# Optimization experiments

Hardware: AMD Instinct MI355X
Metric: run time of the kernel (lower is better)

## Reference

```python
import jax, jax.numpy as jnp
import numpy as np

NPG = 400          # nodes per graph (CC400 atlas ROIs)
B = 512            # graphs per batch
N = B * NPG        # total nodes
EPG = 6400         # edges per graph (avg degree 16)
E = B * EPG
F_IN = 200         # node feature dim
H = 64             # hidden_channels
C = 2              # num_classes


def _lin(k, fi, fo):
    return jax.random.normal(k, (fi, fo), jnp.float32) / np.sqrt(fi)


def setup_inputs() -> dict:
    key = jax.random.key(0)
    ks = jax.random.split(key, 16)
    # intra-graph edges: local src/dst in [0, NPG) plus per-graph offset
    g = jnp.repeat(jnp.arange(B, dtype=jnp.int32), EPG)
    src = jax.random.randint(ks[0], (E,), 0, NPG, dtype=jnp.int32) + g * NPG
    dst = jax.random.randint(ks[1], (E,), 0, NPG, dtype=jnp.int32) + g * NPG
    edge_index = jnp.stack([src, dst])  # [2, E]
    x = jax.random.normal(ks[2], (N, F_IN), jnp.float32)
    return dict(
        x=x, edge_index=edge_index, npg=NPG,
        # SAGEConv i: out = lin_l(mean_agg) + lin_r(x); lin_l carries the bias
        W1l=_lin(ks[3], F_IN, H), W1r=_lin(ks[4], F_IN, H), b1=jnp.zeros((H,), jnp.float32),
        W2l=_lin(ks[5], H, H), W2r=_lin(ks[6], H, H), b2=jnp.zeros((H,), jnp.float32),
        W3l=_lin(ks[7], H, H), W3r=_lin(ks[8], H, H), b3=jnp.zeros((H,), jnp.float32),
        # SAGPooling score GNN = GraphConv(H, 1): lin_rel(sum_agg) + lin_root(x)
        Wpr=_lin(ks[9], H, 1), bpr=jnp.zeros((1,), jnp.float32), Wpo=_lin(ks[10], H, 1),
        # final classifier
        Wlin=_lin(ks[11], H, C), blin=jnp.zeros((C,), jnp.float32),
    )


def reference(x, edge_index, npg, W1l, W1r, b1, W2l, W2r, b2, W3l, W3r, b3,
              Wpr, bpr, Wpo, Wlin, blin):
    n = x.shape[0]
    src, dst = edge_index[0], edge_index[1]

    deg = jax.ops.segment_sum(jnp.ones((src.shape[0],), x.dtype), dst, num_segments=n)
    inv_deg = 1.0 / jnp.maximum(deg, 1.0)  # [n]

    def sage(h, Wl, Wr, b):
        # mean aggregation over incoming edges, then lin_l(agg)+b + lin_r(h)
        agg = jax.ops.segment_sum(h[src], dst, num_segments=n) * inv_deg[:, None]
        return agg @ Wl + b + h @ Wr

    x1 = jax.nn.relu(sage(x, W1l, W1r, b1))
    x2 = jax.nn.relu(sage(x1, W2l, W2r, b2)) + x1
    x3 = jax.nn.relu(sage(x2, W3l, W3r, b3)) + x2

    # SAGPooling score via GraphConv (add aggregation)
    score = (jax.ops.segment_sum(x3[src], dst, num_segments=n) @ Wpr + bpr
             + x3 @ Wpo)[:, 0]  # [n]

    nb = n // npg            # number of graphs
    k = npg // 2             # ratio = 0.5, uniform graph sizes
    vals, idx = jax.lax.top_k(score.reshape(nb, npg), k)       # [nb, k]
    flat_idx = (jnp.arange(nb, dtype=idx.dtype)[:, None] * npg + idx).reshape(-1)
    xp = x3[flat_idx] * jnp.tanh(vals.reshape(-1))[:, None]    # [nb*k, H]

    pooled = xp.reshape(nb, k, -1).mean(axis=1)                # global_mean_pool
    logits = pooled @ Wlin + blin
    return jax.nn.log_softmax(logits, axis=1)
```

## Files before the change

### kernel.cpp

```cpp
#include <hip/hip_runtime.h>
#include <hip/hip_bf16.h>
#include <math.h>

#define F_IN 200
#define HDIM 64
#define NPG  400
#define EPG  6400
#define KSEL 200

typedef __attribute__((ext_vector_type(4))) float f32x4;
typedef __attribute__((ext_vector_type(8))) short s16x8;

__device__ __forceinline__ void gload_lds16(const void* g, void* l) {
    __builtin_amdgcn_global_load_lds(
        (const __attribute__((address_space(1))) void*)g,
        (__attribute__((address_space(3))) void*)l, 16, 0, 0);
}

__device__ __forceinline__ unsigned int bf16_rne(float x) {
    unsigned int b = __float_as_uint(x);
    return (b + 0x7FFFu + ((b >> 16) & 1u)) >> 16;
}

__device__ __forceinline__ void split8(f32x4 v0, f32x4 v1, s16x8& h, s16x8& l) {
    float x[8] = {v0.x, v0.y, v0.z, v0.w, v1.x, v1.y, v1.z, v1.w};
#pragma unroll
    for (int j = 0; j < 8; j++) {
        unsigned int hb = bf16_rne(x[j]);
        float hf = __uint_as_float(hb << 16);
        float r = x[j] - hf;
        unsigned int lb = bf16_rne(r);
        h[j] = (short)hb;
        l[j] = (short)lb;
    }
}

__global__ void pack_wf(const float* __restrict__ Wl, const float* __restrict__ Wr,
                        short* __restrict__ WF, int K, int KC) {
    int idx = blockIdx.x * blockDim.x + threadIdx.x;
    if (idx >= KC * 4096) return;
    int j    = idx & 7;
    int lane = (idx >> 3) & 63;
    int nf   = (idx >> 9) & 7;
    int kc   = idx >> 12;
    int k = kc * 32 + (lane >> 4) * 8 + j;
    int n = nf * 16 + (lane & 15);
    float v = 0.f;
    if (k < K) v = (n < 64) ? Wl[k * 64 + n] : Wr[k * 64 + (n - 64)];
    unsigned int hb = bf16_rne(v);
    float hf = __uint_as_float(hb << 16);
    unsigned int lb = bf16_rne(v - hf);
    WF[(size_t)((kc * 8 + nf) * 2 + 0) * 512 + lane * 8 + j] = (short)hb;
    WF[(size_t)((kc * 8 + nf) * 2 + 1) * 512 + lane * 8 + j] = (short)lb;
}

__global__ void pack_wf4(const float* __restrict__ Wl, const float* __restrict__ Wr,
                         short* __restrict__ WF) {
    int idx = blockIdx.x * blockDim.x + threadIdx.x;
    if (idx >= 4 * 2048) return;
    int j    = idx & 7;
    int lane = (idx >> 3) & 63;
    int nf   = (idx >> 9) & 3;
    int kc   = idx >> 11;
    int k = kc * 32 + (lane >> 4) * 8 + j;
    int n = nf * 16 + (lane & 15);
    float v = (k < 64) ? Wl[k * 64 + n] : Wr[(k - 64) * 64 + n];
    unsigned int hb = bf16_rne(v);
    float hf = __uint_as_float(hb << 16);
    unsigned int lb = bf16_rne(v - hf);
    WF[(size_t)((kc * 4 + nf) * 2 + 0) * 512 + lane * 8 + j] = (short)hb;
    WF[(size_t)((kc * 4 + nf) * 2 + 1) * 512 + lane * 8 + j] = (short)lb;
}

template <int K, int LDX, int KC, int TAIL>
__global__ __launch_bounds__(256) void gemm_lds(const float* __restrict__ X,
                                                const short* __restrict__ WF,
                                                float* __restrict__ O) {
    __shared__ float Xs[2][128 * 32];
    __shared__ short Ws[2][8 * 2 * 512];
    const int tid  = threadIdx.x;
    const int lane = tid & 63;
    const int wave = tid >> 6;
    const size_t rowbase = (size_t)blockIdx.x * 128;
    const f32x4 zero4 = (f32x4){0.f, 0.f, 0.f, 0.f};

    const int srow_off = wave * 32 + (lane >> 3);
    const int sbyte    = 16 * ((lane & 7) ^ (lane >> 3));

#define DMA_CHUNK(b, kc_) {                                                      \
    _Pragma("unroll")                                                            \
    for (int j = 0; j < 4; j++) {                                                \
        const char* xsrc = (const char*)X +                                      \
            (rowbase + srow_off + j * 8) * (size_t)(LDX * 4) + (kc_) * 128 + sbyte; \
        gload_lds16(xsrc, (char*)&Xs[b][0] + wave * 4096 + j * 1024);            \
        const short* wsrc = WF + (size_t)(kc_) * 8192 + wave * 2048 + j * 512 + lane * 8; \
        gload_lds16(wsrc, (char*)&Ws[b][0] + wave * 4096 + j * 1024);            \
    } }

    f32x4 acc[2][8];
#pragma unroll
    for (int m = 0; m < 2; m++)
#pragma unroll
        for (int nf = 0; nf < 8; nf++) acc[m][nf] = zero4;

    DMA_CHUNK(0, 0);
    __syncthreads();

    for (int kc = 0; kc < KC; kc++) {
        const int b = kc & 1;
        if (kc + 1 < KC) DMA_CHUNK(b ^ 1, kc + 1);

        s16x8 ah[2], al[2];
#pragma unroll
        for (int m = 0; m < 2; m++) {
            const int lr = wave * 32 + m * 16 + (lane & 15);
            const int g0 = (lane >> 4) * 2;
            f32x4 v0 = *(const f32x4*)&Xs[b][lr * 32 + 4 * (g0 ^ (lane & 7))];
            f32x4 v1 = *(const f32x4*)&Xs[b][lr * 32 + 4 * ((g0 + 1) ^ (lane & 7))];
            split8(v0, v1, ah[m], al[m]);
        }
#pragma unroll
        for (int nf = 0; nf < 8; nf++) {
            s16x8 wh = *(const s16x8*)&Ws[b][(nf * 2 + 0) * 512 + lane * 8];
            s16x8 wl = *(const s16x8*)&Ws[b][(nf * 2 + 1) * 512 + lane * 8];
#pragma unroll
            for (int m = 0; m < 2; m++) {
                acc[m][nf] = __builtin_amdgcn_mfma_f32_16x16x32_bf16(ah[m], wh, acc[m][nf], 0, 0, 0);
                acc[m][nf] = __builtin_amdgcn_mfma_f32_16x16x32_bf16(al[m], wh, acc[m][nf], 0, 0, 0);
                acc[m][nf] = __builtin_amdgcn_mfma_f32_16x16x32_bf16(ah[m], wl, acc[m][nf], 0, 0, 0);
            }
        }
        __syncthreads();
    }
#undef DMA_CHUNK

    if constexpr (TAIL > 0) {
        s16x8 ah[2], al[2];
#pragma unroll
        for (int m = 0; m < 2; m++) {
            const size_t row = rowbase + wave * 32 + m * 16 + (lane & 15);
            const int k0 = KC * 32 + (lane >> 4) * 8;
            f32x4 v0 = (k0 + 4 <= K) ? *(const f32x4*)&X[row * (size_t)LDX + k0] : zero4;
            f32x4 v1 = (k0 + 8 <= K) ? *(const f32x4*)&X[row * (size_t)LDX + k0 + 4] : zero4;
            split8(v0, v1, ah[m], al[m]);
        }
#pragma unroll
        for (int nf = 0; nf < 8; nf++) {
            s16x8 wh = *(const s16x8*)&WF[(size_t)((KC * 8 + nf) * 2 + 0) * 512 + lane * 8];
            s16x8 wl = *(const s16x8*)&WF[(size_t)((KC * 8 + nf) * 2 + 1) * 512 + lane * 8];
#pragma unroll
            for (int m = 0; m < 2; m++) {
                acc[m][nf] = __builtin_amdgcn_mfma_f32_16x16x32_bf16(ah[m], wh, acc[m][nf], 0, 0, 0);
                acc[m][nf] = __builtin_amdgcn_mfma_f32_16x16x32_bf16(al[m], wh, acc[m][nf], 0, 0, 0);
                acc[m][nf] = __builtin_amdgcn_mfma_f32_16x16x32_bf16(ah[m], wl, acc[m][nf], 0, 0, 0);
            }
        }
    }

    float* cs0 = &Xs[0][wave * 1024];
    float* cs1 = &Xs[1][wave * 1024];
#pragma unroll
    for (int m = 0; m < 2; m++) {
        const int scol = lane & 15;
        const int srow = (lane >> 4) * 4;
#pragma unroll
        for (int nf = 0; nf < 8; nf++)
#pragma unroll
            for (int r = 0; r < 4; r++) {
                int cr = srow + r;
                float* p = (cr < 8) ? cs0 + cr * 128 : cs1 + (cr - 8) * 128;
                p[nf * 16 + scol] = acc[m][nf][r];
            }
#pragma unroll
        for (int ps = 0; ps < 8; ps++) {
            int row = ps * 2 + (lane >> 5);
            const float* p = (row < 8) ? cs0 + row * 128 : cs1 + (row - 8) * 128;
            f32x4 v = *(const f32x4*)&p[(lane & 31) * 4];
            *(f32x4*)&O[(rowbase + wave * 32 + m * 16 + row) * 128 + (lane & 31) * 4] = v;
        }
    }
}

__global__ __launch_bounds__(256) void combine_ss(
    const float* __restrict__ M, const float* __restrict__ H,
    const short* __restrict__ WF, const float* __restrict__ bias,
    const float* __restrict__ resid, float* __restrict__ P)
{
    __shared__ float Xs[4][64 * 32];
    const int tid  = threadIdx.x;
    const int lane = tid & 63;
    const int wave = tid >> 6;
    const size_t rowbase = (size_t)blockIdx.x * 64;
    const s16x8* WFv = (const s16x8*)WF;

#pragma unroll
    for (int c = 0; c < 4; c++) {
        const float* srcbuf = (c < 2) ? M : H;
#pragma unroll
        for (int i = 0; i < 2; i++) {
            int rr = i * 8 + (lane >> 3);
            int jj = (lane & 7) ^ (rr & 7);
            const char* src = (const char*)(srcbuf + (rowbase + wave * 16 + rr) * 64)
                              + (c & 1) * 128 + jj * 16;
            gload_lds16(src, (char*)&Xs[c][0] + wave * 2048 + i * 1024 + lane * 16);
        }
    }
    __syncthreads();

    f32x4 acc[4];
#pragma unroll
    for (int nf = 0; nf < 4; nf++) acc[nf] = (f32x4){0.f, 0.f, 0.f, 0.f};

    const int r = lane & 15;
    const int j0 = (lane >> 4) * 2;
#pragma unroll
    for (int kc = 0; kc < 4; kc++) {
        const float* abase = &Xs[kc][wave * 512 + r * 32];
        f32x4 v0 = *(const f32x4*)&abase[((j0    ) ^ (r & 7)) * 4];
        f32x4 v1 = *(const f32x4*)&abase[((j0 + 1) ^ (r & 7)) * 4];
        s16x8 ah, al;
        split8(v0, v1, ah, al);
        const s16x8* wb = WFv + (size_t)(kc * 4) * 128 + lane;
#pragma unroll
        for (int nf = 0; nf < 4; nf++) {
            s16x8 wh = wb[nf * 128];
            s16x8 wl = wb[nf * 128 + 64];
            acc[nf] = __builtin_amdgcn_mfma_f32_16x16x32_bf16(ah, wh, acc[nf], 0, 0, 0);
            acc[nf] = __builtin_amdgcn_mfma_f32_16x16x32_bf16(al, wh, acc[nf], 0, 0, 0);
            acc[nf] = __builtin_amdgcn_mfma_f32_16x16x32_bf16(ah, wl, acc[nf], 0, 0, 0);
        }
    }

    {
        float* cs0 = &Xs[0][wave * 512];
        float* cs1 = &Xs[1][wave * 512];
        const int scol = lane & 15;
        const int srow = (lane >> 4) * 4;
#pragma unroll
        for (int nf = 0; nf < 4; nf++)
#pragma unroll
            for (int ri = 0; ri < 4; ri++) {
                int cr = srow + ri;
                float* p = (cr < 8) ? cs0 + cr * 64 : cs1 + (cr - 8) * 64;
                p[nf * 16 + scol] = acc[nf][ri];
            }
#pragma unroll
        for (int i = 0; i < 4; i++) {
            int row = i * 4 + (lane >> 4);
            int col = (lane & 15) * 4;
            const float* p = (row < 8) ? cs0 + row * 64 : cs1 + (row - 8) * 64;
            f32x4 v = *(const f32x4*)&p[col];
            size_t grow = rowbase + wave * 16 + row;
            f32x4 bb = *(const f32x4*)&bias[col];
            f32x4 rr = *(const f32x4*)&resid[grow * 64 + col];
            f32x4 o;
#pragma unroll
            for (int q = 0; q < 4; q++) o[q] = fmaxf(v[q] + bb[q], 0.f) + rr[q];
            *(f32x4*)&P[grow * 64 + col] = o;
        }
    }
}

__global__ __launch_bounds__(256) void csr_build(
    const int* __restrict__ esrc, const int* __restrict__ edst,
    int* __restrict__ csr_src, int* __restrict__ rowptr,
    int* __restrict__ degs, float* __restrict__ invdeg)
{
    __shared__ int cnt[NPG];
    __shared__ int off[NPG];
    __shared__ int cur[NPG];
    const int g = blockIdx.x, tid = threadIdx.x;
    const int ebase = g * EPG, nodebase = g * NPG;
    for (int i = tid; i < NPG; i += 256) cnt[i] = 0;
    __syncthreads();
    for (int e = tid; e < EPG; e += 256)
        atomicAdd(&cnt[edst[ebase + e] - nodebase], 1);
    __syncthreads();
    if (tid == 0) {
        int run = 0;
        for (int i = 0; i < NPG; i++) { off[i] = run; run += cnt[i]; }
    }
    __syncthreads();
    for (int i = tid; i < NPG; i += 256) {
        cur[i] = off[i];
        rowptr[nodebase + i] = off[i];
        degs[nodebase + i] = cnt[i];
        invdeg[nodebase + i] = 1.f / fmaxf((float)cnt[i], 1.f);
    }
    __syncthreads();
    for (int e = tid; e < EPG; e += 256) {
        int ld = edst[ebase + e] - nodebase;
        int p = atomicAdd(&cur[ld], 1);
        csr_src[ebase + p] = esrc[ebase + e] - nodebase;
    }
}

__global__ __launch_bounds__(1024) void agg_lds(
    const float* __restrict__ A,
    const int* __restrict__ csr_src, const int* __restrict__ rowptr,
    const int* __restrict__ degs, const float* __restrict__ invdeg,
    const float* __restrict__ bias,
    float* __restrict__ Xout)
{
    __shared__ float y[NPG * 64];
    __shared__ int   csr_l[EPG];
    const int g = blockIdx.x, tid = threadIdx.x;
    const int ebase = g * EPG, nodebase = g * NPG;

    for (int idx = tid; idx < NPG * 16; idx += 1024) {
        int node = idx >> 4, c4 = (idx & 15) * 4;
        *(float4*)&y[node * 64 + c4] =
            *(const float4*)&A[(size_t)(nodebase + node) * 128 + c4];
    }
    for (int e = tid; e < EPG; e += 1024) csr_l[e] = csr_src[ebase + e];
    __syncthreads();

    const int wave = tid >> 6, lane = tid & 63;
    for (int node = wave; node < NPG; node += 16) {
        const int start = rowptr[nodebase + node];
        const int dg = degs[nodebase + node];
        float acc = 0.f;
        int j = 0;
        for (; j + 4 <= dg; j += 4) {
            int s0 = csr_l[start + j];
            int s1 = csr_l[start + j + 1];
            int s2 = csr_l[start + j + 2];
            int s3 = csr_l[start + j + 3];
            acc += y[s0 * 64 + lane] + y[s1 * 64 + lane]
                 + y[s2 * 64 + lane] + y[s3 * 64 + lane];
        }
        for (; j < dg; j++) acc += y[csr_l[start + j] * 64 + lane];

        float v = acc * invdeg[nodebase + node] + bias[lane]
                + A[(size_t)(nodebase + node) * 128 + 64 + lane];
        Xout[(size_t)(nodebase + node) * 64 + lane] = fmaxf(v, 0.f);
    }
}

__global__ __launch_bounds__(1024) void agg_in(
    const float* __restrict__ H,
    const int* __restrict__ csr_src, const int* __restrict__ rowptr,
    const int* __restrict__ degs, const float* __restrict__ invdeg,
    float* __restrict__ M)
{
    __shared__ float y[NPG * 64];
    __shared__ int   csr_l[EPG];
    const int g = blockIdx.x, tid = threadIdx.x;
    const int ebase = g * EPG, nodebase = g * NPG;

    for (int idx = tid; idx < NPG * 16; idx += 1024) {
        int node = idx >> 4, c4 = (idx & 15) * 4;
        *(float4*)&y[node * 64 + c4] =
            *(const float4*)&H[(size_t)(nodebase + node) * 64 + c4];
    }
    for (int e = tid; e < EPG; e += 1024) csr_l[e] = csr_src[ebase + e];
    __syncthreads();

    const int wave = tid >> 6, lane = tid & 63;
    for (int node = wave; node < NPG; node += 16) {
        const int start = rowptr[nodebase + node];
        const int dg = degs[nodebase + node];
        float acc = 0.f;
        int j = 0;
        for (; j + 4 <= dg; j += 4) {
            int s0 = csr_l[start + j];
            int s1 = csr_l[start + j + 1];
            int s2 = csr_l[start + j + 2];
            int s3 = csr_l[start + j + 3];
            acc += y[s0 * 64 + lane] + y[s1 * 64 + lane]
                 + y[s2 * 64 + lane] + y[s3 * 64 + lane];
        }
        for (; j < dg; j++) acc += y[csr_l[start + j] * 64 + lane];

        M[(size_t)(nodebase + node) * 64 + lane] = acc * invdeg[nodebase + node];
    }
}

__global__ __launch_bounds__(1024) void score_pool3(
    const float* __restrict__ X3,
    const int* __restrict__ esrc, const int* __restrict__ edst,
    const float* __restrict__ Wpr, const float* __restrict__ bpr,
    const float* __restrict__ Wpo,
    const float* __restrict__ Wlin, const float* __restrict__ blin,
    float* __restrict__ out)
{
    __shared__ float y[NPG * 64];
    __shared__ float t0s[NPG], ss[NPG], wsel[NPG];
    __shared__ float wprs[64], wpos[64];
    __shared__ float pp[16 * 64];
    __shared__ float pooled[64];
    __shared__ float lgs[2];
    const int g = blockIdx.x, tid = threadIdx.x;
    const int nodebase = g * NPG, ebase = g * EPG;

    if (tid < 64) { wprs[tid] = Wpr[tid]; wpos[tid] = Wpo[tid]; }
    for (int idx = tid; idx < NPG * 16; idx += 1024) {
        int node = idx >> 4, c4 = (idx & 15) * 4;
        *(float4*)&y[node * 64 + c4] =
            *(const float4*)&X3[(size_t)(nodebase + node) * 64 + c4];
    }
    __syncthreads();

    if (tid < NPG) {
        float a0 = 0.f, a1 = 0.f;
        const float* yr = &y[tid * 64];
#pragma unroll
        for (int i = 0; i < 64; i++) {
            int d = (tid + i) & 63;
            float v = yr[d];
            a0 += v * wprs[d];
            a1 += v * wpos[d];
        }
        t0s[tid] = a0;
        ss[tid] = bpr[0] + a1;
    }
    __syncthreads();
    for (int e = tid; e < EPG; e += 1024) {
        int ls = esrc[ebase + e] - nodebase;
        int ld = edst[ebase + e] - nodebase;
        atomicAdd(&ss[ld], t0s[ls]);
    }
    __syncthreads();
    if (tid < NPG) {
        float si = ss[tid];
        int cnt = 0;
        for (int j = 0; j < NPG; j++) {
            float sj = ss[j];
            cnt += (sj > si) || (sj == si && j < tid);
        }
        wsel[tid] = (cnt < KSEL) ? tanhf(si) * (1.f / KSEL) : 0.f;
    }
    __syncthreads();
    {
        const int d = tid & 63, part = tid >> 6;
        float a = 0.f;
        for (int i = part * 25; i < part * 25 + 25; i++)
            a += wsel[i] * y[i * 64 + d];
        pp[part * 64 + d] = a;
    }
    __syncthreads();
    if (tid < 64) {
        float s = 0.f;
#pragma unroll
        for (int i = 0; i < 16; i++) s += pp[i * 64 + tid];
        pooled[tid] = s;
    }
    __syncthreads();
    if (tid < 2) {
        float l = blin[tid];
        for (int d = 0; d < 64; d++) l += pooled[d] * Wlin[d * 2 + tid];
        lgs[tid] = l;
    }
    __syncthreads();
    if (tid < 2) {
        float m = fmaxf(lgs[0], lgs[1]);
        float lse = m + logf(expf(lgs[0] - m) + expf(lgs[1] - m));
        out[g * 2 + tid] = lgs[tid] - lse;
    }
}

extern "C" void kernel_launch(void* const* d_in, const int* in_sizes, int n_in,
                              void* d_out, int out_size, void* d_ws, size_t ws_size,
                              hipStream_t stream) {
    const float* x    = (const float*)d_in[0];
    const int*   eidx = (const int*)d_in[1];
    const float* W1l  = (const float*)d_in[3];
    const float* W1r  = (const float*)d_in[4];
    const float* b1   = (const float*)d_in[5];
    const float* W2l  = (const float*)d_in[6];
    const float* W2r  = (const float*)d_in[7];
    const float* b2   = (const float*)d_in[8];
    const float* W3l  = (const float*)d_in[9];
    const float* W3r  = (const float*)d_in[10];
    const float* b3   = (const float*)d_in[11];
    const float* Wpr  = (const float*)d_in[12];
    const float* bpr  = (const float*)d_in[13];
    const float* Wpo  = (const float*)d_in[14];
    const float* Wlin = (const float*)d_in[15];
    const float* blin = (const float*)d_in[16];

    const int N = in_sizes[0] / F_IN;
    const int E = in_sizes[1] / 2;
    const int B = N / NPG;
    const int* esrc = eidx;
    const int* edst = eidx + E;

    float* ws = (float*)d_ws;
    float* A      = ws;
    float* P0     = A + (size_t)N * 128;
    float* P1     = P0 + (size_t)N * 64;
    float* Mb     = P1 + (size_t)N * 64;
    float* invdeg = Mb + (size_t)N * 64;
    short* WF1    = (short*)(invdeg + N);
    short* WFc2   = WF1 + 57344;
    short* WFc3   = WFc2 + 16384;
    int*   csr    = (int*)(WFc3 + 16384);
    int*   rowptr = csr + E;
    int*   degs   = rowptr + N;

    pack_wf<<<(7 * 4096 + 255) / 256, 256, 0, stream>>>(W1l, W1r, WF1, 200, 7);
    pack_wf4<<<(4 * 2048 + 255) / 256, 256, 0, stream>>>(W2l, W2r, WFc2);
    pack_wf4<<<(4 * 2048 + 255) / 256, 256, 0, stream>>>(W3l, W3r, WFc3);

    csr_build<<<B, 256, 0, stream>>>(esrc, edst, csr, rowptr, degs, invdeg);

    gemm_lds<200, 200, 6, 8><<<N / 128, 256, 0, stream>>>(x, WF1, A);
    agg_lds<<<B, 1024, 0, stream>>>(A, csr, rowptr, degs, invdeg, b1, P0);

    agg_in<<<B, 1024, 0, stream>>>(P0, csr, rowptr, degs, invdeg, Mb);
    combine_ss<<<N / 64, 256, 0, stream>>>(Mb, P0, WFc2, b2, P0, P1);

    agg_in<<<B, 1024, 0, stream>>>(P1, csr, rowptr, degs, invdeg, Mb);
    combine_ss<<<N / 64, 256, 0, stream>>>(Mb, P1, WFc3, b3, P1, P0);

    score_pool3<<<B, 1024, 0, stream>>>(P0, esrc, edst,
                                        Wpr, bpr, Wpo, Wlin, blin,
                                        (float*)d_out);
}
```

Measured before the change: 464.6 us.

## Fuse mean aggregation and SAGE combine GEMM into one per-graph kernel

Replaces the separate agg_in and combine_ss kernels for layers 2 and 3 with a single layer_m kernel that runs one block per graph. The block loads the graph's features into padded LDS, gathers neighbour means straight into MFMA operand registers, and runs the split-bf16 GEMM with the weights staged in LDS. The aim is to drop the intermediate M buffer round trip through global memory and two kernel launches. In exchange the kernel uses much more LDS per block (about 140KB), which limits occupancy, and each lane now gathers 16 floats per edge rather than one.

Result: slower. 509.1 us (+9.6%).

```diff
diff --git a/kernel.cpp b/kernel.cpp
--- a/kernel.cpp
+++ b/kernel.cpp
@@ -7,6 +7,7 @@
 #define NPG  400
 #define EPG  6400
 #define KSEL 200
+#define YST  66
 
 typedef __attribute__((ext_vector_type(4))) float f32x4;
 typedef __attribute__((ext_vector_type(8))) short s16x8;
@@ -181,82 +182,114 @@
     }
 }
 
-__global__ __launch_bounds__(256) void combine_ss(
-    const float* __restrict__ M, const float* __restrict__ H,
-    const short* __restrict__ WF, const float* __restrict__ bias,
-    const float* __restrict__ resid, float* __restrict__ P)
+__global__ __launch_bounds__(512) void layer_m(
+    const float* __restrict__ H,
+    const short* __restrict__ WFc,
+    const float* __restrict__ bias,
+    const int* __restrict__ csr_src, const int* __restrict__ rowptr,
+    const int* __restrict__ degs, const float* __restrict__ invdeg,
+    float* __restrict__ P)
 {
-    __shared__ float Xs[4][64 * 32];
-    const int tid  = threadIdx.x;
-    const int lane = tid & 63;
-    const int wave = tid >> 6;
-    const size_t rowbase = (size_t)blockIdx.x * 64;
-    const s16x8* WFv = (const s16x8*)WF;
-
-#pragma unroll
-    for (int c = 0; c < 4; c++) {
-        const float* srcbuf = (c < 2) ? M : H;
-#pragma unroll
-        for (int i = 0; i < 2; i++) {
-            int rr = i * 8 + (lane >> 3);
-            int jj = (lane & 7) ^ (rr & 7);
-            const char* src = (const char*)(srcbuf + (rowbase + wave * 16 + rr) * 64)
-                              + (c & 1) * 128 + jj * 16;
-            gload_lds16(src, (char*)&Xs[c][0] + wave * 2048 + i * 1024 + lane * 16);
-        }
-    }
-    __syncthreads();
-
-    f32x4 acc[4];
-#pragma unroll
-    for (int nf = 0; nf < 4; nf++) acc[nf] = (f32x4){0.f, 0.f, 0.f, 0.f};
-
-    const int r = lane & 15;
-    const int j0 = (lane >> 4) * 2;
-#pragma unroll
-    for (int kc = 0; kc < 4; kc++) {
-        const float* abase = &Xs[kc][wave * 512 + r * 32];
-        f32x4 v0 = *(const f32x4*)&abase[((j0    ) ^ (r & 7)) * 4];
-        f32x4 v1 = *(const f32x4*)&abase[((j0 + 1) ^ (r & 7)) * 4];
-        s16x8 ah, al;
-        split8(v0, v1, ah, al);
-        const s16x8* wb = WFv + (size_t)(kc * 4) * 128 + lane;
-#pragma unroll
-        for (int nf = 0; nf < 4; nf++) {
-            s16x8 wh = wb[nf * 128];
-            s16x8 wl = wb[nf * 128 + 64];
-            acc[nf] = __builtin_amdgcn_mfma_f32_16x16x32_bf16(ah, wh, acc[nf], 0, 0, 0);
-            acc[nf] = __builtin_amdgcn_mfma_f32_16x16x32_bf16(al, wh, acc[nf], 0, 0, 0);
-            acc[nf] = __builtin_amdgcn_mfma_f32_16x16x32_bf16(ah, wl, acc[nf], 0, 0, 0);
-        }
-    }
-
-    {
-        float* cs0 = &Xs[0][wave * 512];
-        float* cs1 = &Xs[1][wave * 512];
-        const int scol = lane & 15;
-        const int srow = (lane >> 4) * 4;
-#pragma unroll
-        for (int nf = 0; nf < 4; nf++)
-#pragma unroll
-            for (int ri = 0; ri < 4; ri++) {
-                int cr = srow + ri;
-                float* p = (cr < 8) ? cs0 + cr * 64 : cs1 + (cr - 8) * 64;
-                p[nf * 16 + scol] = acc[nf][ri];
-            }
-#pragma unroll
-        for (int i = 0; i < 4; i++) {
-            int row = i * 4 + (lane >> 4);
-            int col = (lane & 15) * 4;
-            const float* p = (row < 8) ? cs0 + row * 64 : cs1 + (row - 8) * 64;
-            f32x4 v = *(const f32x4*)&p[col];
-            size_t grow = rowbase + wave * 16 + row;
-            f32x4 bb = *(const f32x4*)&bias[col];
-            f32x4 rr = *(const f32x4*)&resid[grow * 64 + col];
-            f32x4 o;
-#pragma unroll
-            for (int q = 0; q < 4; q++) o[q] = fmaxf(v[q] + bb[q], 0.f) + rr[q];
-            *(f32x4*)&P[grow * 64 + col] = o;
+    __shared__ float y[NPG * YST];
+    __shared__ unsigned short csrs[EPG];
+    __shared__ short Ws[16384];
+    __shared__ int rps[NPG];
+    __shared__ float invd[NPG];
+    __shared__ unsigned short dgs[NPG];
+    __shared__ float bs[64];
+
+    const int g = blockIdx.x, tid = threadIdx.x;
+    const int lane = tid & 63, wave = tid >> 6;
+    const int nodebase = g * NPG, ebase = g * EPG;
+
+    for (int idx = tid; idx < NPG * 16; idx += 512) {
+        int node = idx >> 4, c4 = (idx & 15) * 4;
+        *(float4*)&y[node * YST + c4] =
+            *(const float4*)&H[(size_t)(nodebase + node) * 64 + c4];
+    }
+    for (int e = tid; e < EPG; e += 512)
+        csrs[e] = (unsigned short)csr_src[ebase + e];
+    for (int i = tid; i < NPG; i += 512) {
+        rps[i]  = rowptr[nodebase + i];
+        invd[i] = invdeg[nodebase + i];
+        dgs[i]  = (unsigned short)degs[nodebase + i];
+    }
+    for (int i = tid; i < 2048; i += 512)
+        *(s16x8*)&Ws[i * 8] = *(const s16x8*)&WFc[i * 8];
+    if (tid < 64) bs[tid] = bias[tid];
+    __syncthreads();
+
+    const int kq = (lane >> 4) * 8;
+    const f32x4 zero4 = (f32x4){0.f, 0.f, 0.f, 0.f};
+
+    for (int f = wave; f < 25; f += 8) {
+        const int nl = f * 16 + (lane & 15);
+        f32x4 m0a = zero4, m0b = zero4, m1a = zero4, m1b = zero4;
+        {
+            const int start = rps[nl];
+            const int dg = dgs[nl];
+            int j = 0;
+            for (; j + 2 <= dg; j += 2) {
+                int s0 = csrs[start + j];
+                int s1 = csrs[start + j + 1];
+                const float* y0 = &y[s0 * YST];
+                const float* y1 = &y[s1 * YST];
+                m0a += *(const f32x4*)&y0[kq]      + *(const f32x4*)&y1[kq];
+                m0b += *(const f32x4*)&y0[kq + 4]  + *(const f32x4*)&y1[kq + 4];
+                m1a += *(const f32x4*)&y0[32 + kq] + *(const f32x4*)&y1[32 + kq];
+                m1b += *(const f32x4*)&y0[32 + kq + 4] + *(const f32x4*)&y1[32 + kq + 4];
+            }
+            for (; j < dg; j++) {
+                int s = csrs[start + j];
+                const float* yr = &y[s * YST];
+                m0a += *(const f32x4*)&yr[kq];
+                m0b += *(const f32x4*)&yr[kq + 4];
+                m1a += *(const f32x4*)&yr[32 + kq];
+                m1b += *(const f32x4*)&yr[32 + kq + 4];
+            }
+            const float inv = invd[nl];
+            m0a *= inv; m0b *= inv; m1a *= inv; m1b *= inv;
+        }
+        s16x8 ah[4], al[4];
+        split8(m0a, m0b, ah[0], al[0]);
+        split8(m1a, m1b, ah[1], al[1]);
+        {
+            const float* hr = &y[nl * YST];
+            f32x4 h0a = *(const f32x4*)&hr[kq];
+            f32x4 h0b = *(const f32x4*)&hr[kq + 4];
+            f32x4 h1a = *(const f32x4*)&hr[32 + kq];
+            f32x4 h1b = *(const f32x4*)&hr[32 + kq + 4];
+            split8(h0a, h0b, ah[2], al[2]);
+            split8(h1a, h1b, ah[3], al[3]);
+        }
+        f32x4 acc[4];
+#pragma unroll
+        for (int nf = 0; nf < 4; nf++) acc[nf] = zero4;
+#pragma unroll
+        for (int kc = 0; kc < 4; kc++) {
+#pragma unroll
+            for (int nf = 0; nf < 4; nf++) {
+                s16x8 wh = *(const s16x8*)&Ws[((kc * 4 + nf) * 2 + 0) * 512 + lane * 8];
+                s16x8 wl = *(const s16x8*)&Ws[((kc * 4 + nf) * 2 + 1) * 512 + lane * 8];
+                acc[nf] = __builtin_amdgcn_mfma_f32_16x16x32_bf16(ah[kc], wh, acc[nf], 0, 0, 0);
+                acc[nf] = __builtin_amdgcn_mfma_f32_16x16x32_bf16(al[kc], wh, acc[nf], 0, 0, 0);
+                acc[nf] = __builtin_amdgcn_mfma_f32_16x16x32_bf16(ah[kc], wl, acc[nf], 0, 0, 0);
+            }
+        }
+        {
+            const int orow0 = f * 16 + (lane >> 4) * 4;
+            const int oc = lane & 15;
+#pragma unroll
+            for (int nf = 0; nf < 4; nf++) {
+                const int col = nf * 16 + oc;
+                const float bv = bs[col];
+#pragma unroll
+                for (int r = 0; r < 4; r++) {
+                    const int lr = orow0 + r;
+                    float v = fmaxf(acc[nf][r] + bv, 0.f) + y[lr * YST + col];
+                    P[(size_t)(nodebase + lr) * 64 + col] = v;
+                }
+            }
         }
     }
 }
@@ -334,45 +367,6 @@
         float v = acc * invdeg[nodebase + node] + bias[lane]
                 + A[(size_t)(nodebase + node) * 128 + 64 + lane];
         Xout[(size_t)(nodebase + node) * 64 + lane] = fmaxf(v, 0.f);
-    }
-}
-
-__global__ __launch_bounds__(1024) void agg_in(
-    const float* __restrict__ H,
-    const int* __restrict__ csr_src, const int* __restrict__ rowptr,
-    const int* __restrict__ degs, const float* __restrict__ invdeg,
-    float* __restrict__ M)
-{
-    __shared__ float y[NPG * 64];
-    __shared__ int   csr_l[EPG];
-    const int g = blockIdx.x, tid = threadIdx.x;
-    const int ebase = g * EPG, nodebase = g * NPG;
-
-    for (int idx = tid; idx < NPG * 16; idx += 1024) {
-        int node = idx >> 4, c4 = (idx & 15) * 4;
-        *(float4*)&y[node * 64 + c4] =
-            *(const float4*)&H[(size_t)(nodebase + node) * 64 + c4];
-    }
-    for (int e = tid; e < EPG; e += 1024) csr_l[e] = csr_src[ebase + e];
-    __syncthreads();
-
-    const int wave = tid >> 6, lane = tid & 63;
-    for (int node = wave; node < NPG; node += 16) {
-        const int start = rowptr[nodebase + node];
-        const int dg = degs[nodebase + node];
-        float acc = 0.f;
-        int j = 0;
-        for (; j + 4 <= dg; j += 4) {
-            int s0 = csr_l[start + j];
-            int s1 = csr_l[start + j + 1];
-            int s2 = csr_l[start + j + 2];
-            int s3 = csr_l[start + j + 3];
-            acc += y[s0 * 64 + lane] + y[s1 * 64 + lane]
-                 + y[s2 * 64 + lane] + y[s3 * 64 + lane];
-        }
-        for (; j < dg; j++) acc += y[csr_l[start + j] * 64 + lane];
-
-        M[(size_t)(nodebase + node) * 64 + lane] = acc * invdeg[nodebase + node];
     }
 }
 
@@ -489,8 +483,7 @@
     float* A      = ws;
     float* P0     = A + (size_t)N * 128;
     float* P1     = P0 + (size_t)N * 64;
-    float* Mb     = P1 + (size_t)N * 64;
-    float* invdeg = Mb + (size_t)N * 64;
+    float* invdeg = P1 + (size_t)N * 64;
     short* WF1    = (short*)(invdeg + N);
     short* WFc2   = WF1 + 57344;
     short* WFc3   = WFc2 + 16384;
@@ -507,11 +500,9 @@
     gemm_lds<200, 200, 6, 8><<<N / 128, 256, 0, stream>>>(x, WF1, A);
     agg_lds<<<B, 1024, 0, stream>>>(A, csr, rowptr, degs, invdeg, b1, P0);
 
-    agg_in<<<B, 1024, 0, stream>>>(P0, csr, rowptr, degs, invdeg, Mb);
-    combine_ss<<<N / 64, 256, 0, stream>>>(Mb, P0, WFc2, b2, P0, P1);
-
-    agg_in<<<B, 1024, 0, stream>>>(P1, csr, rowptr, degs, invdeg, Mb);
-    combine_ss<<<N / 64, 256, 0, stream>>>(Mb, P1, WFc3, b3, P1, P0);
+    layer_m<<<B, 512, 0, stream>>>(P0, WFc2, b2, csr, rowptr, degs, invdeg, P1);
+
+    layer_m<<<B, 512, 0, stream>>>(P1, WFc3, b3, csr, rowptr, degs, invdeg, P0);
 
     score_pool3<<<B, 1024, 0, stream>>>(P0, esrc, edst,
                                         Wpr, bpr, Wpo, Wlin, blin,
```
